# Optimization experiments

Measured on AMD Instinct MI355X. Metric: run time of the kernel, lower is better.

## Reference

```python
import jax, jax.numpy as jnp
import numpy as np

# Config
V = 32000        # Y_vocab_size
EMB = 512        # decoder_embedding_size
ENC_H = 1024     # encoder_hidden_size
DEC_H = 1024     # decoder_hidden_size
ATT = 512        # attention_size
L = 2            # num_decoder_layers
B, T, S = 32, 64, 128


def setup_inputs() -> dict:
    key = jax.random.key(0)
    ks = jax.random.split(key, 20)
    s = 0.02
    emb = jax.random.normal(ks[3], (V, EMB), jnp.float32) * s
    emb = emb.at[0].set(0.0)  # padding_idx=0 row is zeros
    return {
        "y_decoder_input": jax.random.randint(ks[0], (B, T), 0, V),
        "encoder_outputs": jax.random.normal(ks[1], (B, S, ENC_H), jnp.float32),
        "decoder_init_hidden": jax.random.normal(ks[2], (L, B, DEC_H), jnp.float32),
        "encoder_mask": jnp.ones((B, S), jnp.int32),
        "emb_table": emb,
        "W_enc": jax.random.normal(ks[4], (ATT, ENC_H), jnp.float32) * s,
        "W_dec": jax.random.normal(ks[5], (ATT, DEC_H), jnp.float32) * s,
        "v_w": jax.random.normal(ks[6], (ATT,), jnp.float32) * s,
        "W_ih0": jax.random.normal(ks[7], (DEC_H, EMB + ENC_H), jnp.float32) * s,
        "W_hh0": jax.random.normal(ks[8], (DEC_H, DEC_H), jnp.float32) * s,
        "b_ih0": jax.random.normal(ks[9], (DEC_H,), jnp.float32) * s,
        "b_hh0": jax.random.normal(ks[10], (DEC_H,), jnp.float32) * s,
        "W_ih1": jax.random.normal(ks[11], (DEC_H, DEC_H), jnp.float32) * s,
        "W_hh1": jax.random.normal(ks[12], (DEC_H, DEC_H), jnp.float32) * s,
        "b_ih1": jax.random.normal(ks[13], (DEC_H,), jnp.float32) * s,
        "b_hh1": jax.random.normal(ks[14], (DEC_H,), jnp.float32) * s,
        "fc_w": jax.random.normal(ks[15], (V - 1, DEC_H), jnp.float32) * s,
        "fc_b": jnp.zeros((V - 1,), jnp.float32),
    }


def reference(y_decoder_input, encoder_outputs, decoder_init_hidden, encoder_mask,
              emb_table, W_enc, W_dec, v_w,
              W_ih0, W_hh0, b_ih0, b_hh0, W_ih1, W_hh1, b_ih1, b_hh1,
              fc_w, fc_b):
    embedded = emb_table[y_decoder_input]                       # [B,T,EMB]
    enc_proj = jnp.einsum('bse,ae->bsa', encoder_outputs, W_enc)  # hoisted (same math each step)
    pad_mask = (encoder_mask == 0)                              # [B,S]

    def step(hidden, emb_t):
        prev = hidden[-1]                                       # [B,DEC_H] top layer
        dec_p = prev @ W_dec.T                                  # [B,ATT]
        scores = jnp.tanh(enc_proj + dec_p[:, None, :]) @ v_w   # [B,S]
        scores = jnp.where(pad_mask, jnp.float32(-1e9), scores)
        attn = jax.nn.softmax(scores, axis=-1)                  # [B,S]
        context = jnp.einsum('bs,bse->be', attn, encoder_outputs)  # [B,ENC_H]
        x = jnp.concatenate([emb_t, context], axis=1)           # [B,EMB+ENC_H]
        h0 = jnp.tanh(x @ W_ih0.T + b_ih0 + hidden[0] @ W_hh0.T + b_hh0)
        h1 = jnp.tanh(h0 @ W_ih1.T + b_ih1 + hidden[1] @ W_hh1.T + b_hh1)
        out = h1 @ fc_w.T + fc_b                                # [B,V-1]
        return jnp.stack([h0, h1]), (out, attn)

    _, (outs, attns) = jax.lax.scan(step, decoder_init_hidden,
                                    jnp.swapaxes(embedded, 0, 1))  # scan over T
    outputs = jnp.swapaxes(outs, 0, 1)                          # [B,T,V-1]
    attn_weights = jnp.swapaxes(attns, 0, 1)                    # [B,T,S]
    return outputs, attn_weights
```

## Files before the change

kernel.cpp:

```cpp
#include <hip/hip_runtime.h>

typedef unsigned short u16;
typedef unsigned int u32;
typedef __attribute__((ext_vector_type(8))) short bf16x8;
typedef __attribute__((ext_vector_type(4))) float f32x4;
typedef __attribute__((ext_vector_type(2))) unsigned int u32x2;

#define MFMA_BF16(a,b,c) __builtin_amdgcn_mfma_f32_16x16x32_bf16((a),(b),(c),0,0,0)

__device__ __forceinline__ u16 f2bf(float f) {
  union { float f; u32 u; } v; v.f = f;
  u32 r = v.u + 0x7FFFu + ((v.u >> 16) & 1u);
  return (u16)(r >> 16);
}
__device__ __forceinline__ float bf2f(u16 h) {
  union { u32 u; float f; } v; v.u = ((u32)h) << 16; return v.f;
}
__device__ __forceinline__ float tanh_fast(float x) {
  float e = __expf(2.0f * x);
  return 1.0f - 2.0f / (e + 1.0f);
}
__device__ __forceinline__ float exp2_fast(float x) {
  float r; asm("v_exp_f32 %0, %1" : "=v"(r) : "v"(x)); return r;
}
__device__ __forceinline__ float rcp_fast(float x) {
  float r; asm("v_rcp_f32 %0, %1" : "=v"(r) : "v"(x)); return r;
}

__device__ __forceinline__ void issue_lcoh(bf16x8& v, const u16* p) {
  asm volatile("global_load_dwordx4 %0, %1, off sc0 sc1" : "=v"(v) : "v"(p));
}
__device__ __forceinline__ void vm_wait0() {
  asm volatile("s_waitcnt vmcnt(0)" ::: "memory");
  __builtin_amdgcn_sched_barrier(0);
}
__device__ __forceinline__ void scoh_u32(u32* p, u32 v) {
  asm volatile("global_store_dword %0, %1, off sc0 sc1" :: "v"(p), "v"(v) : "memory");
}
__device__ __forceinline__ void scoh_dx2(u16* p, u32 lo, u32 hi) {
  u32x2 v; v.x = lo; v.y = hi;
  asm volatile("global_store_dwordx2 %0, %1, off sc0 sc1" :: "v"(p), "v"(v) : "memory");
}
__device__ __forceinline__ void scoh_dx4(u16* p, bf16x8 v) {
  asm volatile("global_store_dwordx4 %0, %1, off sc0 sc1" :: "v"(p), "v"(v) : "memory");
}
__device__ __forceinline__ u32 poll_load(const u32* p) {
  u32 v;
  asm volatile("global_load_dword %0, %1, off sc0 sc1\n\ts_waitcnt vmcnt(0)"
               : "=v"(v) : "v"(p) : "memory");
  return v;
}

__device__ __forceinline__ void poll_flags(const u32* base, int P, u32 target) {
  if (target == 0u) return;
  if ((threadIdx.x >> 6) == 0) {
    const int lane = threadIdx.x & 63;
    const u32* s0 = base + (size_t)(lane & (P - 1)) * 32;
    for (;;) {
      u32 v0 = poll_load(s0);
      if (__all(v0 >= target)) break;
      __builtin_amdgcn_s_sleep(1);
    }
  }
  __syncthreads();
  __builtin_amdgcn_sched_barrier(0);
}
__device__ __forceinline__ void post_flag(u32* slot, u32 val) {
  asm volatile("s_waitcnt vmcnt(0)" ::: "memory");
  __syncthreads();
  if (threadIdx.x == 0) scoh_u32(slot, val);
}

__global__ void prep_kernel(
    const float* __restrict__ fcw, const float* __restrict__ enc,
    const float* __restrict__ wenc, const float* __restrict__ wdec,
    const float* __restrict__ wih0, const float* __restrict__ whh0,
    const float* __restrict__ wih1, const float* __restrict__ whh1,
    const float* __restrict__ bih0, const float* __restrict__ bhh0,
    const float* __restrict__ bih1, const float* __restrict__ bhh1,
    const float* __restrict__ emb, const int* __restrict__ yin,
    const float* __restrict__ dih,
    u16* __restrict__ fcwb, u16* __restrict__ encb, u16* __restrict__ wencb,
    u16* __restrict__ wdecb, u16* __restrict__ w0eh, u16* __restrict__ w0ctx,
    u16* __restrict__ w1cat, u16* __restrict__ embbt,
    float* __restrict__ bias0, float* __restrict__ bias1,
    u16* __restrict__ h0buf0, u16* __restrict__ h1buf0)
{
  const float SCL = 2.8853900817779268f;
  const long long total = 44632064LL;
  for (long long i = (long long)blockIdx.x * 256 + threadIdx.x; i < total;
       i += (long long)gridDim.x * 256) {
    if (i < 33554432LL) {
      int r = (int)(i >> 10), c = (int)(i & 1023);
      fcwb[i] = (r < 31999) ? f2bf(fcw[(long long)r * 1024 + c]) : (u16)0;
    } else if (i < 37748736LL) {
      long long j = i - 33554432LL; encb[j] = f2bf(enc[j]);
    } else if (i < 38273024LL) {
      long long j = i - 37748736LL; wencb[j] = f2bf(wenc[j] * SCL);
    } else if (i < 38797312LL) {
      long long j = i - 38273024LL; wdecb[j] = f2bf(wdec[j] * SCL);
    } else if (i < 40370176LL) {
      long long j = i - 38797312LL;
      int r = (int)(j / 1536), c = (int)(j % 1536);
      float v = (c < 512) ? wih0[(long long)r * 1536 + c]
                          : whh0[(long long)r * 1024 + (c - 512)];
      w0eh[j] = f2bf(v);
    } else if (i < 41418752LL) {
      long long j = i - 40370176LL;
      int r = (int)(j >> 10), e = (int)(j & 1023);
      w0ctx[j] = f2bf(wih0[(long long)r * 1536 + 512 + e]);
    } else if (i < 43515904LL) {
      long long j = i - 41418752LL;
      int r = (int)(j >> 11), c = (int)(j & 2047);
      w1cat[j] = f2bf(c < 1024 ? wih1[(r << 10) + c] : whh1[(r << 10) + (c - 1024)]);
    } else if (i < 44564480LL) {
      long long j = i - 43515904LL;
      int bt = (int)(j >> 9), c = (int)(j & 511);
      int y = yin[bt];
      embbt[j] = f2bf(emb[(long long)y * 512 + c]);
    } else if (i < 44565504LL) {
      int j = (int)(i - 44564480LL); bias0[j] = bih0[j] + bhh0[j];
    } else if (i < 44566528LL) {
      int j = (int)(i - 44565504LL); bias1[j] = bih1[j] + bhh1[j];
    } else if (i < 44599296LL) {
      int j = (int)(i - 44566528LL); h0buf0[j] = f2bf(dih[j]);
    } else {
      int j = (int)(i - 44599296LL); h1buf0[j] = f2bf(dih[32768 + j]);
    }
  }
}

__global__ __launch_bounds__(256) void gemm128b(
    const u16* __restrict__ A, const u16* __restrict__ Bm,
    u16* __restrict__ Cv, int K, int ldc, int ntN)
{
  __shared__ u16 As[128 * 32];
  __shared__ u16 Bs[128 * 32];
  const int tid = threadIdx.x;
  const int bid = blockIdx.x;
  const int tM = bid / ntN, tN = bid - tM * ntN;
  const int m0 = tM * 128, n0 = tN * 128;
  const int lane = tid & 63, wid = tid >> 6;
  const int wm = wid >> 1, wn = wid & 1;
  const int srow = tid >> 1, scol = (tid & 1) * 16;

  const u16* gA = A + (size_t)(m0 + srow) * K + scol;
  const u16* gB = Bm + (size_t)(n0 + srow) * K + scol;
  u16* sA = &As[srow * 32 + scol];
  u16* sB = &Bs[srow * 32 + scol];

  f32x4 acc[4][4];
#pragma unroll
  for (int i = 0; i < 4; ++i)
#pragma unroll
    for (int j = 0; j < 4; ++j) acc[i][j] = (f32x4){0, 0, 0, 0};

  const int aoff = (wm * 64 + (lane & 15)) * 32 + ((lane >> 4) << 3);
  const int boff = (wn * 64 + (lane & 15)) * 32 + ((lane >> 4) << 3);

  for (int k0 = 0; k0 < K; k0 += 32) {
    bf16x8 va0 = *(const bf16x8*)(gA + k0);
    bf16x8 va1 = *(const bf16x8*)(gA + k0 + 8);
    bf16x8 vb0 = *(const bf16x8*)(gB + k0);
    bf16x8 vb1 = *(const bf16x8*)(gB + k0 + 8);
    __syncthreads();
    *((bf16x8*)sA) = va0;  *((bf16x8*)(sA + 8)) = va1;
    *((bf16x8*)sB) = vb0;  *((bf16x8*)(sB + 8)) = vb1;
    __syncthreads();
    bf16x8 af[4], bfj[4];
#pragma unroll
    for (int i = 0; i < 4; ++i) af[i] = *(const bf16x8*)&As[aoff + i * 512];
#pragma unroll
    for (int j = 0; j < 4; ++j) bfj[j] = *(const bf16x8*)&Bs[boff + j * 512];
#pragma unroll
    for (int i = 0; i < 4; ++i)
#pragma unroll
      for (int j = 0; j < 4; ++j)
        acc[i][j] = MFMA_BF16(af[i], bfj[j], acc[i][j]);
  }

#pragma unroll
  for (int i = 0; i < 4; ++i) {
#pragma unroll
    for (int j = 0; j < 4; ++j) {
      int row = m0 + wm * 64 + i * 16 + ((lane >> 4) << 2);
      int cc = n0 + wn * 64 + j * 16 + (lane & 15);
#pragma unroll
      for (int jj = 0; jj < 4; ++jj)
        Cv[(size_t)(row + jj) * ldc + cc] = f2bf(acc[i][j][jj]);
    }
  }
}

__global__ __launch_bounds__(512, 1) void decoder_persistent(
    const u16* __restrict__ wdecb, const u16* __restrict__ w0eh,
    const u16* __restrict__ w1cat, const u16* __restrict__ encprojb,
    const u16* __restrict__ encW0T, const u16* __restrict__ embbt,
    const float* __restrict__ bias0, const float* __restrict__ bias1,
    const float* __restrict__ vw, const int* __restrict__ msk,
    const u16* __restrict__ fcwb, const float* __restrict__ fcb,
    u16* __restrict__ partials, u16* __restrict__ attbufB,
    u16* __restrict__ h0buf, u16* __restrict__ h1buf,
    u16* __restrict__ h1all, float* __restrict__ outattn,
    float* __restrict__ outlog, u32* flags)
{
  extern __shared__ char smem[];
  const int tid = threadIdx.x;
  const int bid = blockIdx.x;
  const int lane = tid & 63, wid = tid >> 6;
  const int l15 = lane & 15, l16 = (lane >> 4) << 3;
  const f32x4 zero4 = {0, 0, 0, 0};
  u32* h1flags = flags;
  u32* scflags = flags + 32 * 32;
  u32* h0flags = flags + 64 * 32;

  if (bid < 32) {
    const int n0 = bid * 32;
    u16* w1L = (u16*)smem;
    float* scr = (float*)(smem + 131584);
    u16* h1newL = (u16*)(smem + 147968);
    float* b1L = (float*)(smem + 150016);
    {
      for (int c = tid; c < 8192; c += 512) {
        int r = c >> 8, seg = (c & 255) * 8;
        *(bf16x8*)&w1L[r * 2056 + seg] =
            *(const bf16x8*)&w1cat[(size_t)(n0 + r) * 2048 + seg];
      }
      if (tid < 32) b1L[tid] = bias1[n0 + tid];
      for (int c = tid; c < 1024; c += 512) {
        int b = c >> 5, n = c & 31;
        h1newL[c] = h1buf[(size_t)b * 1024 + n0 + n];
      }
    }
    __syncthreads();
    const int bt = wid >> 2, kq = wid & 3;
    const int ab = bt * 16 + l15;

    for (int t = -1; t < 64; ++t) {
      if (t >= 0) {
        poll_flags(h1flags, 32, (u32)(t + 1));
        const u16* hp = h1buf + (size_t)(t & 1) * 32768;
        f32x4 acc0 = zero4, acc1 = zero4;
        {
          bf16x8 av[8];
#pragma unroll
          for (int ks = 0; ks < 8; ++ks)
            issue_lcoh(av[ks], hp + (size_t)ab * 1024 + kq * 256 + ks * 32 + l16);
          vm_wait0();
#pragma unroll
          for (int ks = 0; ks < 8; ++ks) {
            int kx = 1024 + kq * 256 + ks * 32 + l16;
            acc0 = MFMA_BF16(av[ks], *(const bf16x8*)&w1L[l15 * 2056 + kx], acc0);
            acc1 = MFMA_BF16(av[ks], *(const bf16x8*)&w1L[(16 + l15) * 2056 + kx], acc1);
          }
        }
        poll_flags(h0flags, 64, (u32)(t + 1));
        const u16* hn = h0buf + (size_t)((t + 1) & 1) * 32768;
        {
          bf16x8 av[8];
#pragma unroll
          for (int ks = 0; ks < 8; ++ks)
            issue_lcoh(av[ks], hn + (size_t)ab * 1024 + kq * 256 + ks * 32 + l16);
          vm_wait0();
#pragma unroll
          for (int ks = 0; ks < 8; ++ks) {
            int kx = kq * 256 + ks * 32 + l16;
            acc0 = MFMA_BF16(av[ks], *(const bf16x8*)&w1L[l15 * 2056 + kx], acc0);
            acc1 = MFMA_BF16(av[ks], *(const bf16x8*)&w1L[(16 + l15) * 2056 + kx], acc1);
          }
        }
        *(f32x4*)&scr[((wid * 2 + 0) * 64 + lane) * 4] = acc0;
        *(f32x4*)&scr[((wid * 2 + 1) * 64 + lane) * 4] = acc1;
        __syncthreads();
        {
          int b = tid >> 4, n16 = tid & 15;
          int lanep = (((b & 15) >> 2) << 4) | n16;
          int r = b & 3, btc = b >> 4;
#pragma unroll
          for (int nt = 0; nt < 2; ++nt) {
            int n = nt * 16 + n16;
            float s = b1L[n];
#pragma unroll
            for (int q = 0; q < 4; ++q)
              s += scr[(((btc * 4 + q) * 2 + nt) * 64 + lanep) * 4 + r];
            h1newL[b * 32 + n] = f2bf(tanh_fast(s));
          }
        }
        __syncthreads();
        if (tid < 128) {
          int b = tid >> 2, q = tid & 3;
          bf16x8 v8 = *(const bf16x8*)&h1newL[b * 32 + q * 8];
          scoh_dx4(h1buf + (size_t)((t + 1) & 1) * 32768 + (size_t)b * 1024 + n0 + q * 8, v8);
          scoh_dx4(h1all + ((size_t)b * 64 + t) * 1024 + n0 + q * 8, v8);
        }
      }
      {
#pragma unroll
        for (int bt2 = 0; bt2 < 2; ++bt2) {
          bf16x8 hb = *(const bf16x8*)&h1newL[(bt2 * 16 + l15) * 32 + l16];
#pragma unroll
          for (int i = 0; i < 4; ++i) {
            int at = wid * 4 + i;
            bf16x8 wa = *(const bf16x8*)&wdecb[(size_t)(at * 16 + l15) * 1024 + n0 + l16];
            f32x4 c = MFMA_BF16(wa, hb, zero4);
            int a0 = at * 16 + ((lane >> 4) << 2);
            int bb = bt2 * 16 + l15;
            u32 lo = (u32)f2bf(c[0]) | ((u32)f2bf(c[1]) << 16);
            u32 hi = (u32)f2bf(c[2]) | ((u32)f2bf(c[3]) << 16);
            scoh_dx2(partials + ((size_t)bb * 32 + bid) * 512 + a0, lo, hi);
          }
        }
      }
      post_flag(h1flags + (size_t)bid * 32, (u32)(t + 2));
    }
  } else if (bid < 64) {
    const int b = bid - 32;
    u16* epL = (u16*)smem;
    float* vwL = (float*)(smem + 133120);
    float* red = (float*)(smem + 135168);
    float* decpL = (float*)(smem + 151552);
    float* attF = (float*)(smem + 153600);
    u16* attB = (u16*)(smem + 154112);
    float* eL = (float*)(smem + 154368);
    float* mkL = (float*)(smem + 154880);
    float* sumL = (float*)(smem + 155392);
    {
      for (int c = tid; c < 8192; c += 512)
        *(bf16x8*)&epL[(c >> 6) * 520 + (c & 63) * 8] =
            *(const bf16x8*)&encprojb[((size_t)b * 128 + (c >> 6)) * 512 + (c & 63) * 8];
      vwL[tid] = vw[tid];
      if (tid < 128) mkL[tid] = (float)msk[b * 128 + tid];
    }
    __syncthreads();
    for (int t = 0; t < 64; ++t) {
      poll_flags(h1flags, 32, (u32)(t + 1));
      {
        const int a8 = tid & 63, hg = tid >> 6;
        const int a = a8 * 8;
        bf16x8 w[4];
#pragma unroll
        for (int i = 0; i < 4; ++i)
          issue_lcoh(w[i], partials + ((size_t)b * 32 + hg * 4 + i) * 512 + a);
        vm_wait0();
#pragma unroll
        for (int e = 0; e < 8; ++e)
          red[hg * 512 + a + e] = bf2f((u16)w[0][e]) + bf2f((u16)w[1][e]) +
                                  bf2f((u16)w[2][e]) + bf2f((u16)w[3][e]);
      }
      __syncthreads();
      {
        float s = 0.f;
#pragma unroll
        for (int hg = 0; hg < 8; ++hg) s += red[hg * 512 + tid];
        decpL[tid] = s;
      }
      __syncthreads();
      {
        const int s = tid >> 2, q = tid & 3;
        const u16* ep = &epL[s * 520 + q * 128];
        const float* dp = &decpL[q * 128];
        const float* vv = &vwL[q * 128];
        float a0 = 0.f, a1 = 0.f;
#pragma unroll
        for (int ii = 0; ii < 16; ++ii) {
          int i = (ii + q * 4) & 15;
          bf16x8 ev = *(const bf16x8*)(ep + i * 8);
#pragma unroll
          for (int e = 0; e < 8; e += 2) {
            float x0 = bf2f((u16)ev[e]) + dp[i * 8 + e];
            float x1 = bf2f((u16)ev[e + 1]) + dp[i * 8 + e + 1];
            a0 = fmaf(vv[i * 8 + e],     1.f - 2.f * rcp_fast(exp2_fast(x0) + 1.f), a0);
            a1 = fmaf(vv[i * 8 + e + 1], 1.f - 2.f * rcp_fast(exp2_fast(x1) + 1.f), a1);
          }
        }
        float acc = a0 + a1;
        acc += __shfl_xor(acc, 1);
        acc += __shfl_xor(acc, 2);
        float e = 0.f;
        if (q == 0) { e = (mkL[s] != 0.f) ? __expf(acc) : 0.f; eL[s] = e; }
        float ee = e;
#pragma unroll
        for (int off = 1; off < 64; off <<= 1) ee += __shfl_xor(ee, off);
        if (lane == 0) sumL[wid] = ee;
      }
      __syncthreads();
      {
        float tot = sumL[0] + sumL[1] + sumL[2] + sumL[3] +
                    sumL[4] + sumL[5] + sumL[6] + sumL[7];
        if (tid < 128) {
          float att = (tot > 0.f) ? eL[tid] * rcp_fast(tot) : 0.0078125f;
          attF[tid] = att;
          attB[tid] = f2bf(att);
        }
      }
      __syncthreads();
      if (tid < 32)
        *(f32x4*)(outattn + ((size_t)b * 64 + t) * 128 + tid * 4) = *(const f32x4*)&attF[tid * 4];
      if (tid < 16)
        scoh_dx4(attbufB + (size_t)b * 128 + tid * 8, *(const bf16x8*)&attB[tid * 8]);
      post_flag(scflags + (size_t)b * 32, (u32)(t + 1));
    }
  } else if (bid < 128) {
    const int h = bid - 64, j0 = h * 16;
    u16* e0L = (u16*)smem;
    float* attL = (float*)(smem + 131328);
    float* scrH = (float*)(smem + 147712);
    u16* h0newL = (u16*)(smem + 155904);
    float* b0L = (float*)(smem + 156928);
    {
      for (int c = tid; c < 8192; c += 512) {
        int j = c >> 9, off = (c & 511) * 8;
        *(bf16x8*)&e0L[j * 4104 + off] =
            *(const bf16x8*)&encW0T[(size_t)(j0 + j) * 4096 + off];
      }
      if (tid < 16) b0L[tid] = bias0[j0 + tid];
    }
    __syncthreads();
    const int bt = wid >> 2, kq = wid & 3;
    const int ab = bt * 16 + l15;

    for (int t = 0; t < 64; ++t) {
      poll_flags(h0flags, 64, (u32)t);
      {
        bf16x8 xa[12], wb[12];
        const u16* hp = h0buf + (size_t)(t & 1) * 32768;
#pragma unroll
        for (int ks = 0; ks < 12; ++ks) {
          int kk = kq * 384 + ks * 32;
          if (kk < 512)
            xa[ks] = *(const bf16x8*)&embbt[((size_t)ab * 64 + t) * 512 + kk + l16];
          else
            issue_lcoh(xa[ks], hp + (size_t)ab * 1024 + (kk - 512) + l16);
          wb[ks] = *(const bf16x8*)&w0eh[(size_t)(j0 + l15) * 1536 + kk + l16];
        }
        vm_wait0();
        f32x4 acc = zero4;
#pragma unroll
        for (int ks = 0; ks < 12; ++ks) acc = MFMA_BF16(xa[ks], wb[ks], acc);
        *(f32x4*)&scrH[(wid * 64 + lane) * 4] = acc;
      }
      poll_flags(scflags, 32, (u32)(t + 1));
      {
        bf16x8 v;
        issue_lcoh(v, attbufB + tid * 8);
        vm_wait0();
#pragma unroll
        for (int e = 0; e < 8; ++e) attL[tid * 8 + e] = bf2f((u16)v[e]);
      }
      __syncthreads();
      {
        int b = tid >> 4, j = tid & 15;
        const float* ar = &attL[b * 128];
        float adot = 0.f;
#pragma unroll
        for (int c8 = 0; c8 < 16; ++c8) {
          bf16x8 ev = *(const bf16x8*)&e0L[j * 4104 + b * 128 + c8 * 8];
#pragma unroll
          for (int e = 0; e < 8; ++e) adot = fmaf(ar[c8 * 8 + e], bf2f((u16)ev[e]), adot);
        }
        int lanep = (((b & 15) >> 2) << 4) | j;
        int r = b & 3, btc = b >> 4;
        float s = adot + b0L[j];
#pragma unroll
        for (int q = 0; q < 4; ++q)
          s += scrH[((btc * 4 + q) * 64 + lanep) * 4 + r];
        h0newL[b * 16 + j] = f2bf(tanh_fast(s));
      }
      __syncthreads();
      if (tid < 64) {
        int b = tid >> 1, half = tid & 1;
        scoh_dx4(h0buf + (size_t)((t + 1) & 1) * 32768 + (size_t)b * 1024 + j0 + half * 8,
                 *(const bf16x8*)&h0newL[b * 16 + half * 8]);
      }
      post_flag(h0flags + (size_t)h * 32, (u32)(t + 1));
    }
  } else {
    const int f = bid - 128;
    const int n0g = f * 256;
    u16* aL = (u16*)smem;
    for (int t = 0; t < 64; ++t) {
      if ((tid >> 6) == 0) {
        const u32* s0 = h1flags + (size_t)(lane & 31) * 32;
        for (;;) {
          u32 v0 = poll_load(s0);
          if (__all(v0 >= (u32)(t + 2))) break;
          __builtin_amdgcn_s_sleep(8);
        }
      }
      __syncthreads();
      __builtin_amdgcn_sched_barrier(0);
      {
        int b = tid >> 4, ks = (tid & 15) * 64;
        bf16x8 v[8];
        const u16* src = h1all + ((size_t)b * 64 + t) * 1024 + ks;
#pragma unroll
        for (int i = 0; i < 8; ++i) issue_lcoh(v[i], src + i * 8);
        vm_wait0();
#pragma unroll
        for (int i = 0; i < 8; ++i) *(bf16x8*)&aL[b * 1024 + ks + i * 8] = v[i];
      }
      __syncthreads();
      f32x4 acc00 = zero4, acc01 = zero4, acc10 = zero4, acc11 = zero4;
      const int nt0 = wid * 2;
      const u16* brow0 = fcwb + (size_t)(n0g + (nt0 + 0) * 16 + l15) * 1024;
      const u16* brow1 = fcwb + (size_t)(n0g + (nt0 + 1) * 16 + l15) * 1024;
#pragma unroll 4
      for (int kk = 0; kk < 32; ++kk) {
        int ko = kk * 32 + l16;
        bf16x8 a0 = *(const bf16x8*)&aL[l15 * 1024 + ko];
        bf16x8 a1 = *(const bf16x8*)&aL[(16 + l15) * 1024 + ko];
        bf16x8 b0 = *(const bf16x8*)(brow0 + ko);
        bf16x8 b1 = *(const bf16x8*)(brow1 + ko);
        acc00 = MFMA_BF16(a0, b0, acc00);
        acc10 = MFMA_BF16(a1, b0, acc10);
        acc01 = MFMA_BF16(a0, b1, acc01);
        acc11 = MFMA_BF16(a1, b1, acc11);
      }
      __syncthreads();
      {
        const int rq = (lane >> 4) << 2;
#pragma unroll
        for (int ntl = 0; ntl < 2; ++ntl) {
          int col = n0g + (nt0 + ntl) * 16 + l15;
          if (col < 31999) {
            float bs = fcb[col];
            f32x4 c0 = ntl ? acc01 : acc00;
            f32x4 c1 = ntl ? acc11 : acc10;
#pragma unroll
            for (int j = 0; j < 4; ++j) {
              outlog[(size_t)((rq + j) * 64 + t) * 31999 + col] = c0[j] + bs;
              outlog[(size_t)((16 + rq + j) * 64 + t) * 31999 + col] = c1[j] + bs;
            }
          }
        }
      }
    }
  }
}

extern "C" void kernel_launch(void* const* d_in, const int* in_sizes, int n_in,
                              void* d_out, int out_size, void* d_ws, size_t ws_size,
                              hipStream_t stream)
{
  const int*   yin  = (const int*)d_in[0];
  const float* enc  = (const float*)d_in[1];
  const float* dih  = (const float*)d_in[2];
  const int*   msk  = (const int*)d_in[3];
  const float* emb  = (const float*)d_in[4];
  const float* wenc = (const float*)d_in[5];
  const float* wdec = (const float*)d_in[6];
  const float* vw   = (const float*)d_in[7];
  const float* wih0 = (const float*)d_in[8];
  const float* whh0 = (const float*)d_in[9];
  const float* bih0 = (const float*)d_in[10];
  const float* bhh0 = (const float*)d_in[11];
  const float* wih1 = (const float*)d_in[12];
  const float* whh1 = (const float*)d_in[13];
  const float* bih1 = (const float*)d_in[14];
  const float* bhh1 = (const float*)d_in[15];
  const float* fcw  = (const float*)d_in[16];
  const float* fcb  = (const float*)d_in[17];

  char* ws = (char*)d_ws;
  size_t off = 0;
  auto alloc = [&](size_t bytes) {
    char* p = ws + off; off += (bytes + 255) & ~(size_t)255; return p;
  };
  u16*   fcwb     = (u16*)alloc(33554432ULL * 2);
  u16*   encb     = (u16*)alloc(4194304ULL * 2);
  u16*   wencb    = (u16*)alloc(524288ULL * 2);
  u16*   wdecb    = (u16*)alloc(524288ULL * 2);
  u16*   w0eh     = (u16*)alloc(1572864ULL * 2);
  u16*   w0ctx    = (u16*)alloc(1048576ULL * 2);
  u16*   w1cat    = (u16*)alloc(2097152ULL * 2);
  u16*   embbt    = (u16*)alloc(1048576ULL * 2);
  u16*   encprojb = (u16*)alloc(2097152ULL * 2);
  u16*   encW0T   = (u16*)alloc(4194304ULL * 2);
  u16*   partials = (u16*)alloc(524288ULL * 2);
  u16*   attbufB  = (u16*)alloc(4096ULL * 2);
  u16*   h0buf    = (u16*)alloc(65536ULL * 2);
  u16*   h1buf    = (u16*)alloc(65536ULL * 2);
  u16*   h1all    = (u16*)alloc(2097152ULL * 2);
  float* bias0    = (float*)alloc(1024ULL * 4);
  float* bias1    = (float*)alloc(1024ULL * 4);
  u32*   flags    = (u32*)alloc(16384ULL);
  if (off > ws_size) return;

  float* outlog  = (float*)d_out;
  float* outattn = outlog + 65533952ULL;

  (void)hipMemsetAsync(flags, 0, 16384, stream);

  prep_kernel<<<2048, 256, 0, stream>>>(
      fcw, enc, wenc, wdec, wih0, whh0, wih1, whh1,
      bih0, bhh0, bih1, bhh1, emb, yin, dih,
      fcwb, encb, wencb, wdecb, w0eh, w0ctx, w1cat, embbt, bias0, bias1,
      h0buf, h1buf);

  gemm128b<<<32 * 4, 256, 0, stream>>>(encb, wencb, encprojb, 1024, 512, 4);
  gemm128b<<<8 * 32, 256, 0, stream>>>(w0ctx, encb, encW0T, 1024, 4096, 32);

  (void)hipFuncSetAttribute((const void*)decoder_persistent,
                            hipFuncAttributeMaxDynamicSharedMemorySize, 157184);
  decoder_persistent<<<256, 512, 157184, stream>>>(
      wdecb, w0eh, w1cat, encprojb, encW0T, embbt, bias0, bias1,
      vw, msk, fcwb, fcb, partials, attbufB, h0buf, h1buf, h1all,
      outattn, outlog, flags);
}
```

Baseline: 1.631 ms.

## Batch FC output over two timesteps and tune flag polling sleep

```diff
diff --git a/kernel.cpp b/kernel.cpp
--- a/kernel.cpp
+++ b/kernel.cpp
@@ -51,15 +51,17 @@
   return v;
 }
 
+template <int SLP>
 __device__ __forceinline__ void poll_flags(const u32* base, int P, u32 target) {
   if (target == 0u) return;
   if ((threadIdx.x >> 6) == 0) {
     const int lane = threadIdx.x & 63;
-    const u32* s0 = base + (size_t)(lane & (P - 1)) * 32;
+    const u32* s0 = base + (size_t)lane * 32;
     for (;;) {
-      u32 v0 = poll_load(s0);
+      u32 v0 = 0xFFFFFFFFu;
+      if (lane < P) v0 = poll_load(s0);
       if (__all(v0 >= target)) break;
-      __builtin_amdgcn_s_sleep(1);
+      __builtin_amdgcn_s_sleep(SLP);
     }
   }
   __syncthreads();
@@ -238,7 +240,7 @@
 
     for (int t = -1; t < 64; ++t) {
       if (t >= 0) {
-        poll_flags(h1flags, 32, (u32)(t + 1));
+        poll_flags<4>(h1flags, 32, (u32)(t + 1));
         const u16* hp = h1buf + (size_t)(t & 1) * 32768;
         f32x4 acc0 = zero4, acc1 = zero4;
         {
@@ -254,7 +256,7 @@
             acc1 = MFMA_BF16(av[ks], *(const bf16x8*)&w1L[(16 + l15) * 2056 + kx], acc1);
           }
         }
-        poll_flags(h0flags, 64, (u32)(t + 1));
+        poll_flags<4>(h0flags, 64, (u32)(t + 1));
         const u16* hn = h0buf + (size_t)((t + 1) & 1) * 32768;
         {
           bf16x8 av[8];
@@ -333,7 +335,7 @@
     }
     __syncthreads();
     for (int t = 0; t < 64; ++t) {
-      poll_flags(h1flags, 32, (u32)(t + 1));
+      poll_flags<4>(h1flags, 32, (u32)(t + 1));
       {
         const int a8 = tid & 63, hg = tid >> 6;
         const int a = a8 * 8;
@@ -420,7 +422,7 @@
     const int ab = bt * 16 + l15;
 
     for (int t = 0; t < 64; ++t) {
-      poll_flags(h0flags, 64, (u32)t);
+      poll_flags<4>(h0flags, 64, (u32)t);
       {
         bf16x8 xa[12], wb[12];
         const u16* hp = h0buf + (size_t)(t & 1) * 32768;
@@ -439,7 +441,7 @@
         for (int ks = 0; ks < 12; ++ks) acc = MFMA_BF16(xa[ks], wb[ks], acc);
         *(f32x4*)&scrH[(wid * 64 + lane) * 4] = acc;
       }
-      poll_flags(scflags, 32, (u32)(t + 1));
+      poll_flags<4>(scflags, 32, (u32)(t + 1));
       {
         bf16x8 v;
         issue_lcoh(v, attbufB + tid * 8);
@@ -478,45 +480,45 @@
     const int f = bid - 128;
     const int n0g = f * 256;
     u16* aL = (u16*)smem;
-    for (int t = 0; t < 64; ++t) {
+    for (int tp = 0; tp < 32; ++tp) {
+      const int t0 = tp * 2;
       if ((tid >> 6) == 0) {
-        const u32* s0 = h1flags + (size_t)(lane & 31) * 32;
+        u32 v0;
+        const u32* s0 = h1flags + (size_t)lane * 32;
         for (;;) {
-          u32 v0 = poll_load(s0);
-          if (__all(v0 >= (u32)(t + 2))) break;
-          __builtin_amdgcn_s_sleep(8);
+          v0 = 0xFFFFFFFFu;
+          if (lane < 32) v0 = poll_load(s0);
+          if (__all(v0 >= (u32)(t0 + 3))) break;
+          __builtin_amdgcn_s_sleep(32);
         }
       }
       __syncthreads();
       __builtin_amdgcn_sched_barrier(0);
-      {
-        int b = tid >> 4, ks = (tid & 15) * 64;
-        bf16x8 v[8];
-        const u16* src = h1all + ((size_t)b * 64 + t) * 1024 + ks;
-#pragma unroll
-        for (int i = 0; i < 8; ++i) issue_lcoh(v[i], src + i * 8);
-        vm_wait0();
-#pragma unroll
-        for (int i = 0; i < 8; ++i) *(bf16x8*)&aL[b * 1024 + ks + i * 8] = v[i];
-      }
-      __syncthreads();
-      f32x4 acc00 = zero4, acc01 = zero4, acc10 = zero4, acc11 = zero4;
+      for (int i = tid; i < 8192; i += 512) {
+        int row = i >> 7, koff = (i & 127) * 8;
+        int s = row >> 5, b = row & 31;
+        *(bf16x8*)&aL[row * 1024 + koff] =
+            *(const bf16x8*)&h1all[((size_t)b * 64 + t0 + s) * 1024 + koff];
+      }
+      __syncthreads();
+      f32x4 acc[4][2];
+#pragma unroll
+      for (int mt = 0; mt < 4; ++mt) { acc[mt][0] = zero4; acc[mt][1] = zero4; }
       const int nt0 = wid * 2;
       const u16* brow0 = fcwb + (size_t)(n0g + (nt0 + 0) * 16 + l15) * 1024;
       const u16* brow1 = fcwb + (size_t)(n0g + (nt0 + 1) * 16 + l15) * 1024;
 #pragma unroll 4
       for (int kk = 0; kk < 32; ++kk) {
         int ko = kk * 32 + l16;
-        bf16x8 a0 = *(const bf16x8*)&aL[l15 * 1024 + ko];
-        bf16x8 a1 = *(const bf16x8*)&aL[(16 + l15) * 1024 + ko];
         bf16x8 b0 = *(const bf16x8*)(brow0 + ko);
         bf16x8 b1 = *(const bf16x8*)(brow1 + ko);
-        acc00 = MFMA_BF16(a0, b0, acc00);
-        acc10 = MFMA_BF16(a1, b0, acc10);
-        acc01 = MFMA_BF16(a0, b1, acc01);
-        acc11 = MFMA_BF16(a1, b1, acc11);
-      }
-      __syncthreads();
+#pragma unroll
+        for (int mt = 0; mt < 4; ++mt) {
+          bf16x8 a = *(const bf16x8*)&aL[(mt * 16 + l15) * 1024 + ko];
+          acc[mt][0] = MFMA_BF16(a, b0, acc[mt][0]);
+          acc[mt][1] = MFMA_BF16(a, b1, acc[mt][1]);
+        }
+      }
       {
         const int rq = (lane >> 4) << 2;
 #pragma unroll
@@ -524,16 +526,19 @@
           int col = n0g + (nt0 + ntl) * 16 + l15;
           if (col < 31999) {
             float bs = fcb[col];
-            f32x4 c0 = ntl ? acc01 : acc00;
-            f32x4 c1 = ntl ? acc11 : acc10;
-#pragma unroll
-            for (int j = 0; j < 4; ++j) {
-              outlog[(size_t)((rq + j) * 64 + t) * 31999 + col] = c0[j] + bs;
-              outlog[(size_t)((16 + rq + j) * 64 + t) * 31999 + col] = c1[j] + bs;
+#pragma unroll
+            for (int mt = 0; mt < 4; ++mt) {
+#pragma unroll
+              for (int j = 0; j < 4; ++j) {
+                int grow = mt * 16 + rq + j;
+                int b = grow & 31, s = grow >> 5;
+                outlog[(size_t)((b * 64) + t0 + s) * 31999 + col] = acc[mt][ntl][j] + bs;
+              }
             }
           }
         }
       }
+      __syncthreads();
     }
   }
 }
```

After: 1.648 ms. About the same (+1.0%).
